# Kernel optimization log

Hardware: AMD Instinct MI355X
Metric: run time of the kernel (lower is better)

The kernel has to match this reference:

```python
import jax, jax.numpy as jnp
import numpy as np

B, T, E = 8, 1048576, 8
C, K, S = 128, 512, 512


def setup_inputs() -> dict:
    key = jax.random.key(0)
    k1, k2, k3, k4, k5 = jax.random.split(key, 5)
    fan = 1.0 / np.sqrt(E * K)  # torch Conv1d default init range
    z = jax.random.normal(k1, (B, T, E), dtype=jnp.float32)
    W1 = jax.random.uniform(k2, (C, E, K), dtype=jnp.float32, minval=-fan, maxval=fan)
    b1 = jax.random.uniform(k3, (C,), dtype=jnp.float32, minval=-fan, maxval=fan)
    W2 = jax.random.uniform(k4, (C, E, K), dtype=jnp.float32, minval=-fan, maxval=fan)
    b2 = jax.random.uniform(k5, (C,), dtype=jnp.float32, minval=-fan, maxval=fan)
    return {"z": z, "W1": W1, "b1": b1, "W2": W2, "b2": b2}


def _conv1d(x_bct, w_oik, b_o):
    # x: (B, E, T), w: (C, E, K), stride S, VALID padding -> (B, C, L)
    y = jax.lax.conv_general_dilated(
        x_bct, w_oik, window_strides=(S,), padding="VALID",
        dimension_numbers=("NCH", "OIH", "NCH"))
    return y + b_o[None, :, None]


def reference(z, W1, b1, W2, b2):
    zt = jnp.transpose(z, (0, 2, 1))          # (B, E, T)
    c1 = _conv1d(zt, W1, b1)                  # (B, C, L)
    c2 = _conv1d(zt, W2, b2)
    g = c1 * jax.nn.sigmoid(c2)               # gated conv
    return jnp.max(g, axis=-1)                # global max-over-time -> (B, C)
```

## Files before the change

### kernel.cpp

```cpp
#include <hip/hip_runtime.h>
#include <hip/hip_bf16.h>
#include <stdint.h>

typedef __attribute__((ext_vector_type(8))) short short8;
typedef __attribute__((ext_vector_type(4))) float f32x4;
typedef __attribute__((ext_vector_type(4))) unsigned int uint4v;

#define KKTOT 4096
#define NTILES 64
#define BM 64
#define BK 64
#define NN 256

typedef const __attribute__((address_space(1))) unsigned int* gas_ptr;
typedef __attribute__((address_space(3))) unsigned int* las_ptr;

__device__ __forceinline__ void gload_lds16(const void* g, void* l) {
  __builtin_amdgcn_global_load_lds((gas_ptr)g, (las_ptr)l, 16, 0, 0);
}

__device__ __forceinline__ unsigned pack_bf2(float a, float b) {
  __hip_bfloat162 h = __float22bfloat162_rn(make_float2(a, b));
  union { __hip_bfloat162 h2; unsigned u; } cv; cv.h2 = h;
  return cv.u;
}

__global__ void pack_w(const float* __restrict__ W1, const float* __restrict__ W2,
                       __hip_bfloat16* __restrict__ WB) {
  int idx = blockIdx.x * 256 + threadIdx.x;
  int j  = idx & 63;
  int n  = (idx >> 6) & 255;
  int kt = idx >> 14;
  int c  = n >> 1;
  const float* W = (n & 1) ? W2 : W1;
  int kk = kt * 64 + j;
  int k = kk >> 3, e = kk & 7;
  float v = W[(c * 8 + e) * 512 + k];
  WB[(size_t)kt * 16384 + n * 64 + (j ^ ((n & 7) << 3))] = __float2bfloat16(v);
}

__global__ __launch_bounds__(512, 2) void gemm_gate(
    const float* __restrict__ z, const __hip_bfloat16* __restrict__ WB,
    const float* __restrict__ b1, const float* __restrict__ b2,
    float* __restrict__ partial) {
  __shared__ __align__(16) __hip_bfloat16 As[2][BM * BK];
  __shared__ __align__(16) __hip_bfloat16 Bs[2][NN * BK];

  const int t = threadIdx.x;
  const int l = t & 63;
  const int w = t >> 6;
  const int wm = w >> 2;
  const int wn = w & 3;
  const int kgrp = l >> 4;
  const int lrow = l & 15;
  const int bid = blockIdx.x;
  const size_t m0 = (size_t)bid * BM;

  const int arow = t >> 3;
  const int aseg = t & 7;
  const float* asrc_base = z + (m0 + arow) * (size_t)KKTOT + aseg * 8;
  const int aoff = arow * 128 + ((aseg ^ (arow & 7)) << 4);

  f32x4 acc[2][4];
#pragma unroll
  for (int i = 0; i < 2; ++i)
#pragma unroll
    for (int j = 0; j < 4; ++j) acc[i][j] = (f32x4)0.0f;

  {
    const float4 f0 = *(const float4*)(asrc_base);
    const float4 f1 = *(const float4*)(asrc_base + 4);
    uint4v pk;
    pk.x = pack_bf2(f0.x, f0.y); pk.y = pack_bf2(f0.z, f0.w);
    pk.z = pack_bf2(f1.x, f1.y); pk.w = pack_bf2(f1.z, f1.w);
    *(uint4v*)((char*)&As[0][0] + aoff) = pk;
    const char* gsrc = (const char*)WB;
#pragma unroll
    for (int r = 0; r < 4; ++r) {
      int o = t * 16 + r * 8192;
      gload_lds16(gsrc + o, (char*)&Bs[0][0] + o);
    }
  }
  __syncthreads();

  for (int kt = 0; kt < NTILES; ++kt) {
    const int cur = kt & 1;
    const bool has_next = (kt + 1 < NTILES);
    float4 f0, f1;
    if (has_next) {
      const float* s = asrc_base + (size_t)(kt + 1) * BK;
      f0 = *(const float4*)(s);
      f1 = *(const float4*)(s + 4);
      const char* gsrc = (const char*)WB + (size_t)(kt + 1) * 32768;
      char* bdst = (char*)&Bs[cur ^ 1][0];
#pragma unroll
      for (int r = 0; r < 4; ++r) {
        int o = t * 16 + r * 8192;
        gload_lds16(gsrc + o, bdst + o);
      }
    }
    const char* abase = (const char*)&As[cur][0];
    const char* bbase = (const char*)&Bs[cur][0];
    short8 af[2][2], bfr[4][2];
#pragma unroll
    for (int i = 0; i < 2; ++i) {
      const int r = wm * 32 + i * 16 + lrow;
      const int sw = (r & 7) << 4;
#pragma unroll
      for (int h = 0; h < 2; ++h)
        af[i][h] = *(const short8*)(abase + r * 128 + (((h * 4 + kgrp) << 4) ^ sw));
    }
#pragma unroll
    for (int j = 0; j < 4; ++j) {
      const int r = wn * 64 + j * 16 + lrow;
      const int sw = (r & 7) << 4;
#pragma unroll
      for (int h = 0; h < 2; ++h)
        bfr[j][h] = *(const short8*)(bbase + r * 128 + (((h * 4 + kgrp) << 4) ^ sw));
    }
#pragma unroll
    for (int i = 0; i < 2; ++i)
#pragma unroll
      for (int j = 0; j < 4; ++j)
#pragma unroll
        for (int h = 0; h < 2; ++h)
          acc[i][j] = __builtin_amdgcn_mfma_f32_16x16x32_bf16(
              af[i][h], bfr[j][h], acc[i][j], 0, 0, 0);
    if (has_next) {
      uint4v pk;
      pk.x = pack_bf2(f0.x, f0.y); pk.y = pack_bf2(f0.z, f0.w);
      pk.z = pack_bf2(f1.x, f1.y); pk.w = pack_bf2(f1.z, f1.w);
      *(uint4v*)((char*)&As[cur ^ 1][0] + aoff) = pk;
    }
    __syncthreads();
  }

  const int col = lrow;
  float gmax[4];
#pragma unroll
  for (int j = 0; j < 4; ++j) {
    const int c = wn * 32 + j * 8 + (col >> 1);
    const float vb1 = b1[c], vb2 = b2[c];
    float gm = -3.4e38f;
#pragma unroll
    for (int i = 0; i < 2; ++i) {
#pragma unroll
      for (int rr = 0; rr < 4; ++rr) {
        float v = acc[i][j][rr];
        float p = __shfl_xor(v, 1, 64);
        float c1 = (col & 1) ? p : v;
        float c2 = (col & 1) ? v : p;
        c1 += vb1; c2 += vb2;
        float g = c1 * (1.0f / (1.0f + __expf(-c2)));
        gm = fmaxf(gm, g);
      }
    }
    gm = fmaxf(gm, __shfl_xor(gm, 16, 64));
    gm = fmaxf(gm, __shfl_xor(gm, 32, 64));
    gmax[j] = gm;
  }
  if ((l & 1) == 0 && l < 16) {
    float* pp = partial + ((size_t)bid * 2 + wm) * 128;
#pragma unroll
    for (int j = 0; j < 4; ++j)
      pp[wn * 32 + j * 8 + (l >> 1)] = gmax[j];
  }
}

__global__ void reduce_max(const float* __restrict__ partial, float* __restrict__ out) {
  int idx = blockIdx.x * 256 + threadIdx.x;
  if (idx >= 1024) return;
  int b = idx >> 7, c = idx & 127;
  float m = -3.4e38f;
#pragma unroll 8
  for (int p = 0; p < 64; ++p)
    m = fmaxf(m, partial[(size_t)(b * 64 + p) * 128 + c]);
  out[idx] = m;
}

extern "C" void kernel_launch(void* const* d_in, const int* in_sizes, int n_in,
                              void* d_out, int out_size, void* d_ws, size_t ws_size,
                              hipStream_t stream) {
  const float* z  = (const float*)d_in[0];
  const float* W1 = (const float*)d_in[1];
  const float* b1 = (const float*)d_in[2];
  const float* W2 = (const float*)d_in[3];
  const float* b2 = (const float*)d_in[4];
  float* out = (float*)d_out;

  __hip_bfloat16* WB = (__hip_bfloat16*)d_ws;
  float* partial = (float*)((char*)d_ws + 2 * 1024 * 1024);

  pack_w<<<4096, 256, 0, stream>>>(W1, W2, WB);
  gemm_gate<<<256, 512, 0, stream>>>(z, WB, b1, b2, partial);
  reduce_max<<<4, 256, 0, stream>>>(partial, out);
}
```

Before: 439.6 us.

## Load A fragments directly to registers, 4-stage B pipeline, split N across blocks

```diff
diff --git a/kernel.cpp b/kernel.cpp
--- a/kernel.cpp
+++ b/kernel.cpp
@@ -4,13 +4,9 @@
 
 typedef __attribute__((ext_vector_type(8))) short short8;
 typedef __attribute__((ext_vector_type(4))) float f32x4;
-typedef __attribute__((ext_vector_type(4))) unsigned int uint4v;
 
-#define KKTOT 4096
-#define NTILES 64
-#define BM 64
-#define BK 64
-#define NN 256
+#define NT 64
+#define NBUF 4
 
 typedef const __attribute__((address_space(1))) unsigned int* gas_ptr;
 typedef __attribute__((address_space(3))) unsigned int* las_ptr;
@@ -20,46 +16,54 @@
 }
 
 __device__ __forceinline__ unsigned pack_bf2(float a, float b) {
-  __hip_bfloat162 h = __float22bfloat162_rn(make_float2(a, b));
-  union { __hip_bfloat162 h2; unsigned u; } cv; cv.h2 = h;
+  union { __hip_bfloat162 h2; unsigned u; } cv;
+  cv.h2 = __float22bfloat162_rn(make_float2(a, b));
   return cv.u;
+}
+
+__device__ __forceinline__ short8 pack8(const f32x4& a, const f32x4& b) {
+  union { unsigned u[4]; short8 s; } cv;
+  cv.u[0] = pack_bf2(a.x, a.y); cv.u[1] = pack_bf2(a.z, a.w);
+  cv.u[2] = pack_bf2(b.x, b.y); cv.u[3] = pack_bf2(b.z, b.w);
+  return cv.s;
 }
 
 __global__ void pack_w(const float* __restrict__ W1, const float* __restrict__ W2,
                        __hip_bfloat16* __restrict__ WB) {
   int idx = blockIdx.x * 256 + threadIdx.x;
-  int j  = idx & 63;
-  int n  = (idx >> 6) & 255;
-  int kt = idx >> 14;
-  int c  = n >> 1;
+  int kk = idx & 4095, n = idx >> 12;
+  int k = kk >> 3, e = kk & 7, c = n >> 1;
   const float* W = (n & 1) ? W2 : W1;
-  int kk = kt * 64 + j;
-  int k = kk >> 3, e = kk & 7;
-  float v = W[(c * 8 + e) * 512 + k];
-  WB[(size_t)kt * 16384 + n * 64 + (j ^ ((n & 7) << 3))] = __float2bfloat16(v);
+  WB[(size_t)n * 4096 + kk] = __float2bfloat16(W[(c * 8 + e) * 512 + k]);
 }
 
-__global__ __launch_bounds__(512, 2) void gemm_gate(
+__global__ __launch_bounds__(256, 2) void gemm_gate(
     const float* __restrict__ z, const __hip_bfloat16* __restrict__ WB,
     const float* __restrict__ b1, const float* __restrict__ b2,
     float* __restrict__ partial) {
-  __shared__ __align__(16) __hip_bfloat16 As[2][BM * BK];
-  __shared__ __align__(16) __hip_bfloat16 Bs[2][NN * BK];
+  __shared__ __align__(16) char Bs[NBUF][16384];
 
   const int t = threadIdx.x;
-  const int l = t & 63;
-  const int w = t >> 6;
-  const int wm = w >> 2;
-  const int wn = w & 3;
-  const int kgrp = l >> 4;
-  const int lrow = l & 15;
-  const int bid = blockIdx.x;
-  const size_t m0 = (size_t)bid * BM;
+  const int l = t & 63, w = t >> 6;
+  const int wm = w >> 1, wn = w & 1;
+  const int lr = l & 15, lk = l >> 4;
 
-  const int arow = t >> 3;
-  const int aseg = t & 7;
-  const float* asrc_base = z + (m0 + arow) * (size_t)KKTOT + aseg * 8;
-  const int aoff = arow * 128 + ((aseg ^ (arow & 7)) << 4);
+  const int h = blockIdx.x;
+  const int logical = (h & 7) * 64 + (h >> 3);
+  const int mb = logical >> 1, nh = logical & 1;
+
+  const int rowbase = mb * 64 + wm * 32;
+  const int nbase = nh * 128;
+
+  const char* bsrc[4];
+#pragma unroll
+  for (int r = 0; r < 4; ++r) {
+    int col = r * 32 + (t >> 3);
+    int inner = ((t & 7) * 16) ^ ((col & 7) << 4);
+    bsrc[r] = (const char*)(WB + (size_t)(nbase + col) * 4096) + inner;
+  }
+
+  const char* abase = (const char*)(z + (size_t)(rowbase + lr) * 4096 + lk * 8);
 
   f32x4 acc[2][4];
 #pragma unroll
@@ -67,89 +71,86 @@
 #pragma unroll
     for (int j = 0; j < 4; ++j) acc[i][j] = (f32x4)0.0f;
 
-  {
-    const float4 f0 = *(const float4*)(asrc_base);
-    const float4 f1 = *(const float4*)(asrc_base + 4);
-    uint4v pk;
-    pk.x = pack_bf2(f0.x, f0.y); pk.y = pack_bf2(f0.z, f0.w);
-    pk.z = pack_bf2(f1.x, f1.y); pk.w = pack_bf2(f1.z, f1.w);
-    *(uint4v*)((char*)&As[0][0] + aoff) = pk;
-    const char* gsrc = (const char*)WB;
+  f32x4 acur[8], anext[8];
+
 #pragma unroll
-    for (int r = 0; r < 4; ++r) {
-      int o = t * 16 + r * 8192;
-      gload_lds16(gsrc + o, (char*)&Bs[0][0] + o);
+  for (int kt0 = 0; kt0 < 3; ++kt0)
+#pragma unroll
+    for (int r = 0; r < 4; ++r)
+      gload_lds16(bsrc[r] + (size_t)kt0 * 128, &Bs[kt0][r * 4096 + t * 16]);
+#pragma unroll
+  for (int mi = 0; mi < 2; ++mi)
+#pragma unroll
+    for (int ks = 0; ks < 2; ++ks)
+#pragma unroll
+      for (int hf = 0; hf < 2; ++hf)
+        acur[mi * 4 + ks * 2 + hf] =
+            *(const f32x4*)(abase + ((size_t)mi * 16 * 4096 + ks * 32 + hf * 4) * 4);
+  asm volatile("s_waitcnt vmcnt(0)" ::: "memory");
+  __builtin_amdgcn_s_barrier();
+
+  const int swz = (lr & 7) << 4;
+#pragma unroll 1
+  for (int kt = 0; kt < NT; ++kt) {
+    if (kt + 3 < NT) {
+      char* dst = (char*)Bs[(kt + 3) & 3];
+#pragma unroll
+      for (int r = 0; r < 4; ++r)
+        gload_lds16(bsrc[r] + (size_t)(kt + 3) * 128, dst + r * 4096 + t * 16);
     }
-  }
-  __syncthreads();
-
-  for (int kt = 0; kt < NTILES; ++kt) {
-    const int cur = kt & 1;
-    const bool has_next = (kt + 1 < NTILES);
-    float4 f0, f1;
-    if (has_next) {
-      const float* s = asrc_base + (size_t)(kt + 1) * BK;
-      f0 = *(const float4*)(s);
-      f1 = *(const float4*)(s + 4);
-      const char* gsrc = (const char*)WB + (size_t)(kt + 1) * 32768;
-      char* bdst = (char*)&Bs[cur ^ 1][0];
+    if (kt + 1 < NT) {
 #pragma unroll
-      for (int r = 0; r < 4; ++r) {
-        int o = t * 16 + r * 8192;
-        gload_lds16(gsrc + o, bdst + o);
-      }
+      for (int mi = 0; mi < 2; ++mi)
+#pragma unroll
+        for (int ks = 0; ks < 2; ++ks)
+#pragma unroll
+          for (int hf = 0; hf < 2; ++hf)
+            anext[mi * 4 + ks * 2 + hf] = *(const f32x4*)(
+                abase + ((size_t)(kt + 1) * 64 + (size_t)mi * 16 * 4096 + ks * 32 + hf * 4) * 4);
     }
-    const char* abase = (const char*)&As[cur][0];
-    const char* bbase = (const char*)&Bs[cur][0];
-    short8 af[2][2], bfr[4][2];
+    short8 af[2][2];
 #pragma unroll
-    for (int i = 0; i < 2; ++i) {
-      const int r = wm * 32 + i * 16 + lrow;
-      const int sw = (r & 7) << 4;
+    for (int mi = 0; mi < 2; ++mi)
 #pragma unroll
-      for (int h = 0; h < 2; ++h)
-        af[i][h] = *(const short8*)(abase + r * 128 + (((h * 4 + kgrp) << 4) ^ sw));
+      for (int ks = 0; ks < 2; ++ks)
+        af[mi][ks] = pack8(acur[mi * 4 + ks * 2], acur[mi * 4 + ks * 2 + 1]);
+    const char* bb = (const char*)Bs[kt & 3];
+    short8 bf[4][2];
+#pragma unroll
+    for (int nj = 0; nj < 4; ++nj) {
+      const int col = wn * 64 + nj * 16 + lr;
+#pragma unroll
+      for (int ks = 0; ks < 2; ++ks)
+        bf[nj][ks] = *(const short8*)(bb + col * 128 + ((ks * 64 + lk * 16) ^ swz));
     }
 #pragma unroll
-    for (int j = 0; j < 4; ++j) {
-      const int r = wn * 64 + j * 16 + lrow;
-      const int sw = (r & 7) << 4;
+    for (int mi = 0; mi < 2; ++mi)
 #pragma unroll
-      for (int h = 0; h < 2; ++h)
-        bfr[j][h] = *(const short8*)(bbase + r * 128 + (((h * 4 + kgrp) << 4) ^ sw));
+      for (int nj = 0; nj < 4; ++nj)
+#pragma unroll
+        for (int ks = 0; ks < 2; ++ks)
+          acc[mi][nj] = __builtin_amdgcn_mfma_f32_16x16x32_bf16(
+              af[mi][ks], bf[nj][ks], acc[mi][nj], 0, 0, 0);
+    if (kt + 1 < NT) {
+#pragma unroll
+      for (int i = 0; i < 8; ++i) acur[i] = anext[i];
     }
-#pragma unroll
-    for (int i = 0; i < 2; ++i)
-#pragma unroll
-      for (int j = 0; j < 4; ++j)
-#pragma unroll
-        for (int h = 0; h < 2; ++h)
-          acc[i][j] = __builtin_amdgcn_mfma_f32_16x16x32_bf16(
-              af[i][h], bfr[j][h], acc[i][j], 0, 0, 0);
-    if (has_next) {
-      uint4v pk;
-      pk.x = pack_bf2(f0.x, f0.y); pk.y = pack_bf2(f0.z, f0.w);
-      pk.z = pack_bf2(f1.x, f1.y); pk.w = pack_bf2(f1.z, f1.w);
-      *(uint4v*)((char*)&As[cur ^ 1][0] + aoff) = pk;
-    }
-    __syncthreads();
+    __builtin_amdgcn_s_barrier();
   }
 
-  const int col = lrow;
-  float gmax[4];
 #pragma unroll
-  for (int j = 0; j < 4; ++j) {
-    const int c = wn * 32 + j * 8 + (col >> 1);
+  for (int nj = 0; nj < 4; ++nj) {
+    const int c = nh * 64 + wn * 32 + nj * 8 + (lr >> 1);
     const float vb1 = b1[c], vb2 = b2[c];
     float gm = -3.4e38f;
 #pragma unroll
-    for (int i = 0; i < 2; ++i) {
+    for (int mi = 0; mi < 2; ++mi) {
 #pragma unroll
       for (int rr = 0; rr < 4; ++rr) {
-        float v = acc[i][j][rr];
+        float v = acc[mi][nj][rr];
         float p = __shfl_xor(v, 1, 64);
-        float c1 = (col & 1) ? p : v;
-        float c2 = (col & 1) ? v : p;
+        float c1 = (lr & 1) ? p : v;
+        float c2 = (lr & 1) ? v : p;
         c1 += vb1; c2 += vb2;
         float g = c1 * (1.0f / (1.0f + __expf(-c2)));
         gm = fmaxf(gm, g);
@@ -157,13 +158,8 @@
     }
     gm = fmaxf(gm, __shfl_xor(gm, 16, 64));
     gm = fmaxf(gm, __shfl_xor(gm, 32, 64));
-    gmax[j] = gm;
-  }
-  if ((l & 1) == 0 && l < 16) {
-    float* pp = partial + ((size_t)bid * 2 + wm) * 128;
-#pragma unroll
-    for (int j = 0; j < 4; ++j)
-      pp[wn * 32 + j * 8 + (l >> 1)] = gmax[j];
+    if ((l < 16) && !(l & 1))
+      partial[(size_t)(mb * 2 + wm) * 128 + c] = gm;
   }
 }
 
@@ -173,8 +169,8 @@
   int b = idx >> 7, c = idx & 127;
   float m = -3.4e38f;
 #pragma unroll 8
-  for (int p = 0; p < 64; ++p)
-    m = fmaxf(m, partial[(size_t)(b * 64 + p) * 128 + c]);
+  for (int g = 0; g < 64; ++g)
+    m = fmaxf(m, partial[(size_t)(b * 64 + g) * 128 + c]);
   out[idx] = m;
 }
 
@@ -192,6 +188,6 @@
   float* partial = (float*)((char*)d_ws + 2 * 1024 * 1024);
 
   pack_w<<<4096, 256, 0, stream>>>(W1, W2, WB);
-  gemm_gate<<<256, 512, 0, stream>>>(z, WB, b1, b2, partial);
+  gemm_gate<<<512, 256, 0, stream>>>(z, WB, b1, b2, partial);
   reduce_max<<<4, 256, 0, stream>>>(partial, out);
 }
```

Measured after the change: 464.0 us. 1.06x slower.
